# Kernel optimization log

Hardware: AMD Instinct MI355X
Metric: run time of the kernel (lower is better)

The kernel has to match this reference:

```python
import jax, jax.numpy as jnp
import numpy as np
from jax import lax

B, C, O, H, W = 4, 64, 64, 128, 128
K, PAD = 3, 1


def conv3x3(x, w, b):
    # standard 3x3 conv, stride 1, pad 1, NCHW / OIHW
    y = lax.conv_general_dilated(x, w, window_strides=(1, 1),
                                 padding=((PAD, PAD), (PAD, PAD)))
    return y + b[None, :, None, None]


def deform_conv(x, offset, w, b):
    # torchvision DeformConv2d (v1, 1 offset group): offset is [B, 2*K*K, H, W]
    # with (dy, dx) interleaved per kernel tap; sample pos = p0 + p_k + offset.
    Bn, Cn, Hn, Wn = x.shape
    off = offset.reshape(Bn, K * K, 2, Hn, Wn)
    ky, kx = jnp.meshgrid(jnp.arange(K), jnp.arange(K), indexing='ij')
    ky = ky.reshape(-1).astype(x.dtype)  # [9]
    kx = kx.reshape(-1).astype(x.dtype)
    base_y = jnp.arange(Hn, dtype=x.dtype)[None, None, :, None] - PAD + ky[None, :, None, None]
    base_x = jnp.arange(Wn, dtype=x.dtype)[None, None, None, :] - PAD + kx[None, :, None, None]
    py = base_y + off[:, :, 0]  # [B,9,H,W]
    px = base_x + off[:, :, 1]
    y0 = jnp.floor(py)
    x0 = jnp.floor(px)
    ly = py - y0  # bilinear fractional weights
    lx = px - x0
    y0i = y0.astype(jnp.int32)
    x0i = x0.astype(jnp.int32)
    xflat = x.reshape(Bn, Cn, Hn * Wn)

    def gather(yi, xi):
        valid = ((yi >= 0) & (yi < Hn) & (xi >= 0) & (xi < Wn)).astype(x.dtype)
        idx = (jnp.clip(yi, 0, Hn - 1) * Wn + jnp.clip(xi, 0, Wn - 1)).reshape(Bn, 1, -1)
        v = jnp.take_along_axis(xflat, idx, axis=2).reshape(Bn, Cn, K * K, Hn, Wn)
        return v * valid[:, None]  # zero padding outside image

    v00 = gather(y0i, x0i)
    v01 = gather(y0i, x0i + 1)
    v10 = gather(y0i + 1, x0i)
    v11 = gather(y0i + 1, x0i + 1)
    wy = ly[:, None]  # [B,1,9,H,W]
    wx = lx[:, None]
    samp = (v00 * (1 - wy) * (1 - wx) + v01 * (1 - wy) * wx
            + v10 * wy * (1 - wx) + v11 * wy * wx)  # [B,C,9,H,W]
    out = jnp.einsum('bckhw,ock->bohw', samp, w.reshape(w.shape[0], Cn, K * K))
    return out + b[None, :, None, None]


def setup_inputs() -> dict:
    key = jax.random.key(0)
    ks = jax.random.split(key, 16)
    n = lambda k, s, sc: jax.random.normal(k, s, jnp.float32) * sc
    inp = {
        'ref': n(ks[0], (B, C, H, W), 1.0),
        'nbr': n(ks[1], (B, C, H, W), 1.0),
        # offset convs: small weights so predicted offsets stay O(1) pixels
        'w_off1': n(ks[2], (18, 2 * C, 3, 3), 0.01), 'b_off1': n(ks[3], (18,), 0.01),
        'w_d1': n(ks[4], (O, C, 3, 3), 0.05), 'b_d1': n(ks[5], (O,), 0.05),
        'w_off2': n(ks[6], (18, 2 * O, 3, 3), 0.01), 'b_off2': n(ks[7], (18,), 0.01),
        'w_d2': n(ks[8], (O, O, 3, 3), 0.05), 'b_d2': n(ks[9], (O,), 0.05),
        'w_off3': n(ks[10], (18, 2 * O, 3, 3), 0.01), 'b_off3': n(ks[11], (18,), 0.01),
        'w_d3': n(ks[12], (O, O, 3, 3), 0.05), 'b_d3': n(ks[13], (O,), 0.05),
    }
    return inp


def reference(ref, nbr, w_off1, b_off1, w_d1, b_d1, w_off2, b_off2, w_d2, b_d2,
              w_off3, b_off3, w_d3, b_d3):
    offset1 = conv3x3(jnp.concatenate([ref, nbr], axis=1), w_off1, b_off1)
    d1 = deform_conv(nbr, offset1, w_d1, b_d1)
    offset2 = conv3x3(jnp.concatenate([ref, d1], axis=1), w_off2, b_off2)
    d2 = deform_conv(d1, offset2, w_d2, b_d2)
    offset3 = conv3x3(jnp.concatenate([ref, d2], axis=1), w_off3, b_off3)
    d3 = deform_conv(d2, offset3, w_d3, b_d3)
    return d3
```

## Files before the change

### kernel.cpp

```cpp
#include <hip/hip_runtime.h>
#include <hip/hip_bf16.h>

#define BB 4
#define CC 64
#define HH 128
#define WW 128
#define HW (HH * WW)
#define TOTPIX (BB * HW)

typedef short bf16x8 __attribute__((ext_vector_type(8)));
typedef float f32x4 __attribute__((ext_vector_type(4)));

static __device__ __forceinline__ short f2bf(float f) {
  __hip_bfloat16 h = __float2bfloat16(f);
  return __builtin_bit_cast(short, h);
}
static __device__ __forceinline__ float bf2f(short s) {
  unsigned int u = ((unsigned int)(unsigned short)s) << 16;
  return __builtin_bit_cast(float, u);
}

static __device__ __forceinline__ void stage1k(const short* g, short* lds) {
  __builtin_amdgcn_global_load_lds(
      (const __attribute__((address_space(1))) unsigned int*)g,
      (__attribute__((address_space(3))) unsigned int*)lds, 16, 0, 0);
}

__global__ __launch_bounds__(256) void cast_nhwc_kernel(
    const float* __restrict__ a, const float* __restrict__ b,
    short* __restrict__ oa, short* __restrict__ ob) {
  __shared__ float tile[64][68];
  const int bid = blockIdx.x;
  const int bb = bid >> 8;
  const int hw0 = (bid & 255) * 64;
  const int t = threadIdx.x;
  for (int s = 0; s < 2; s++) {
    const float* src = s ? b : a;
    short* dst = s ? ob : oa;
    if (s) __syncthreads();
    {
      const int lp = t & 15;
      for (int c = (t >> 4); c < 64; c += 16) {
        float4 v = *(const float4*)&src[((size_t)(bb * 64 + c)) * HW + hw0 + lp * 4];
        *(float4*)&tile[c][lp * 4] = v;
      }
    }
    __syncthreads();
    {
      const int px = t >> 2;
      const int seg = t & 3;
      bf16x8 s0, s1;
#pragma unroll
      for (int i = 0; i < 8; i++) s0[i] = f2bf(tile[seg * 16 + i][px]);
#pragma unroll
      for (int i = 0; i < 8; i++) s1[i] = f2bf(tile[seg * 16 + 8 + i][px]);
      short* dp = dst + ((size_t)(bid * 64 + px)) * 64 + seg * 16;
      *(bf16x8*)dp = s0;
      *(bf16x8*)(dp + 8) = s1;
    }
  }
}

__global__ __launch_bounds__(256) void prep_weights_all(
    const float* __restrict__ wd1, const float* __restrict__ wo1,
    short* __restrict__ wtd1, short* __restrict__ wtoff1,
    const float* __restrict__ wd2, const float* __restrict__ wo2,
    short* __restrict__ wtd2, short* __restrict__ wtoff2,
    const float* __restrict__ wd3, const float* __restrict__ wo3,
    short* __restrict__ wtd3, short* __restrict__ wtoff3) {
  const int s = blockIdx.x / 144;
  const float* wd = (s == 0) ? wd1 : (s == 1) ? wd2 : wd3;
  const float* wo = (s == 0) ? wo1 : (s == 1) ? wo2 : wo3;
  short* wtd = (s == 0) ? wtd1 : (s == 1) ? wtd2 : wtd3;
  short* wtoff = (s == 0) ? wtoff1 : (s == 1) ? wtoff2 : wtoff3;
  const int i = (blockIdx.x % 144) * 256 + threadIdx.x;
  const int j = i & 7, l = (i >> 3) & 63, f = i >> 9;
  {
    int ot = f & 3, cf = (f >> 2) & 1, k = f >> 3;
    int o = ot * 16 + (l & 15), c = cf * 32 + (l >> 4) * 8 + j;
    wtd[i] = f2bf(wd[(o * 64 + c) * 9 + k]);
  }
  {
    int ot = f & 1, ks = f >> 1;
    int cs = ks & 3, k = ks >> 2;
    int o = ot * 16 + (l & 15), c = cs * 32 + (l >> 4) * 8 + j;
    wtoff[i] = (o < 18) ? f2bf(wo[(o * 128 + c) * 9 + k]) : (short)0;
  }
}

__global__ __launch_bounds__(256, 4) void off_tile_kernel(
    const short* __restrict__ ref, const short* __restrict__ x2,
    const short* __restrict__ wtoff, const float* __restrict__ bias,
    float* __restrict__ out) {
  __shared__ short tile[2 * 6 * 24 * 64];
  int bid = blockIdx.x;
  bid = (bid & 7) * (gridDim.x >> 3) + (bid >> 3);
  const int tid = threadIdx.x;
  const int l = tid & 63;
  const int g = __builtin_amdgcn_readfirstlane(tid >> 6);
  const int col = l & 15, quad = l >> 4;
  const int b = bid >> 8;
  const int rem = bid & 255;
  const int h0 = (rem >> 3) * 4;
  const int w0 = (rem & 7) * 16;
  const int oy = h0 - 1, ox = w0 - 1;
  const int h = h0 + g, w = w0 + col;
  const int pix = ((b << 7) + h) * WW + w;

  const short* srcs[2] = {ref + (size_t)b * (HW * 64), x2 + (size_t)b * (HW * 64)};

  {
    const int tc = l >> 3;
    const int m = l & 7;
#pragma unroll
    for (int i = 0; i < 9; i++) {
      const int idx = g + i * 4;
      const int t = idx / 18;
      const int rr = (idx % 18) / 3, seg = idx % 3;
      const int iy = min(max(oy + rr, 0), HH - 1);
      const int tcol = seg * 8 + tc;
      const int ix = min(max(ox + tcol, 0), WW - 1);
      const int sc = (m - tcol) & 7;
      stage1k(srcs[t] + (((iy << 7) + ix) << 6) + sc * 8,
              &tile[((t * 6 + rr) * 24 + seg * 8) << 6]);
    }
  }

  f32x4 acc0 = {0.f, 0.f, 0.f, 0.f}, acc1 = {0.f, 0.f, 0.f, 0.f};
  const bf16x8* wp = (const bf16x8*)wtoff + l;

  __syncthreads();

#pragma unroll
  for (int k = 0; k < 9; k++) {
    const int ky = k / 3, kx = k - ky * 3;
    const int hh = h + ky - 1, ww2 = w + kx - 1;
    const bool valid = (hh >= 0) & (hh < HH) & (ww2 >= 0) & (ww2 < WW);
    const int tr = g + ky;
    const int tcx = col + kx;
#pragma unroll
    for (int cs = 0; cs < 4; cs++) {
      const int t = cs >> 1;
      const int chunk = (cs & 1) * 4 + quad;
      bf16x8 v = *(const bf16x8*)&tile[(((t * 6 + tr) * 24 + tcx) << 6) +
                                       (((chunk + tcx) & 7) << 3)];
      if (!valid) v = (bf16x8)(short)0;
      const int f = (k * 4 + cs) * 2;
      acc0 = __builtin_amdgcn_mfma_f32_16x16x32_bf16(wp[f * 64], v, acc0, 0, 0, 0);
      acc1 = __builtin_amdgcn_mfma_f32_16x16x32_bf16(wp[(f + 1) * 64], v, acc1, 0, 0, 0);
    }
  }

#pragma unroll
  for (int r = 0; r < 4; r++)
    out[(quad * 4 + r) * TOTPIX + pix] = acc0[r] + bias[quad * 4 + r];
  if (quad == 0) {
    out[16 * TOTPIX + pix] = acc1[0] + bias[16];
    out[17 * TOTPIX + pix] = acc1[1] + bias[17];
  }
}

#define TH 16
#define TWP 24
__global__ __launch_bounds__(512, 4) void deform_tile_kernel(
    const short* __restrict__ x, const float* __restrict__ off,
    const short* __restrict__ wtd, const float* __restrict__ bias,
    float* __restrict__ outf, short* __restrict__ outb) {
  __shared__ short tile[TH * TWP * 64];
  int bid = blockIdx.x;
  bid = (bid & 7) * (gridDim.x >> 3) + (bid >> 3);
  const int tid = threadIdx.x;
  const int l = tid & 63;
  const int wv = __builtin_amdgcn_readfirstlane(tid >> 6);
  const int col = l & 15, quad = l >> 4;
  const int b = bid >> 7;
  const int rem = bid & 127;
  const int h0 = (rem >> 3) * 8;
  const int w0 = (rem & 7) * 16;
  const int oy = h0 - 4, ox = w0 - 4;
  const int h = h0 + wv, w = w0 + col;
  const int pix = ((b << 7) + h) * WW + w;

  const short* xb = x + (size_t)b * (HW * 64);

  {
    const int tc = ((l >> 3) & 7);
    const int m = l & 7;
#pragma unroll
    for (int i = 0; i < 6; i++) {
      const int idx = wv + i * 8;
      const int r = idx / 3, seg = idx % 3;
      const int iy = min(max(oy + r, 0), HH - 1);
      const int tcol = seg * 8 + tc;
      const int ix = min(max(ox + tcol, 0), WW - 1);
      const int sc = (m - tcol) & 7;
      stage1k(xb + (((iy << 7) + ix) << 6) + sc * 8,
              &tile[((r * TWP + seg * 8) << 6)]);
    }
  }

  float offv[18];
#pragma unroll
  for (int j = 0; j < 18; j++) offv[j] = off[j * TOTPIX + pix];

  f32x4 acc[4];
#pragma unroll
  for (int ot = 0; ot < 4; ot++)
#pragma unroll
    for (int r = 0; r < 4; r++) acc[ot][r] = 0.f;

  const int c0g = quad * 8;
  const bf16x8* wp = (const bf16x8*)wtd + l;

  __syncthreads();

#pragma unroll
  for (int k = 0; k < 9; k++) {
    const int ky = k / 3, kx = k - ky * 3;
    const float py = (float)(h - 1 + ky) + offv[2 * k];
    const float pxx = (float)(w - 1 + kx) + offv[2 * k + 1];
    const float y0f = floorf(py), x0f = floorf(pxx);
    const float ly = py - y0f, lx = pxx - x0f;
    const int y0 = (int)y0f, x0 = (int)x0f;
    const int y1 = y0 + 1, x1 = x0 + 1;
    float w00 = (1.f - ly) * (1.f - lx), w01 = (1.f - ly) * lx;
    float w10 = ly * (1.f - lx), w11 = ly * lx;
    if (y0 < 0 || y0 >= HH) { w00 = 0.f; w01 = 0.f; }
    if (y1 < 0 || y1 >= HH) { w10 = 0.f; w11 = 0.f; }
    if (x0 < 0 || x0 >= WW) { w00 = 0.f; w10 = 0.f; }
    if (x1 < 0 || x1 >= WW) { w01 = 0.f; w11 = 0.f; }
    const int cy0 = min(max(y0, 0), HH - 1), cy1 = min(max(y1, 0), HH - 1);
    const int cx0 = min(max(x0, 0), WW - 1), cx1 = min(max(x1, 0), WW - 1);

    const int ty0 = cy0 - oy, ty1 = cy1 - oy;
    const int tx0 = cx0 - ox, tx1 = cx1 - ox;
    const bool intile = (ty0 >= 0) & (ty1 < TH) & (tx0 >= 0) & (tx1 < TWP);

    bf16x8 v00a, v00b, v01a, v01b, v10a, v10b, v11a, v11b;
    if (__builtin_amdgcn_ballot_w64(intile) == ~0ull) {
      const int p00 = ((ty0 * TWP + tx0) << 6);
      const int p01 = ((ty0 * TWP + tx1) << 6);
      const int p10 = ((ty1 * TWP + tx0) << 6);
      const int p11 = ((ty1 * TWP + tx1) << 6);
      v00a = *(const bf16x8*)&tile[p00 + (((quad + tx0) & 7) << 3)];
      v00b = *(const bf16x8*)&tile[p00 + (((quad + 4 + tx0) & 7) << 3)];
      v01a = *(const bf16x8*)&tile[p01 + (((quad + tx1) & 7) << 3)];
      v01b = *(const bf16x8*)&tile[p01 + (((quad + 4 + tx1) & 7) << 3)];
      v10a = *(const bf16x8*)&tile[p10 + (((quad + tx0) & 7) << 3)];
      v10b = *(const bf16x8*)&tile[p10 + (((quad + 4 + tx0) & 7) << 3)];
      v11a = *(const bf16x8*)&tile[p11 + (((quad + tx1) & 7) << 3)];
      v11b = *(const bf16x8*)&tile[p11 + (((quad + 4 + tx1) & 7) << 3)];
    } else {
      const int p00 = ((cy0 * WW + cx0) << 6) + c0g;
      const int p01 = ((cy0 * WW + cx1) << 6) + c0g;
      const int p10 = ((cy1 * WW + cx0) << 6) + c0g;
      const int p11 = ((cy1 * WW + cx1) << 6) + c0g;
      v00a = *(const bf16x8*)(xb + p00);
      v00b = *(const bf16x8*)(xb + p00 + 32);
      v01a = *(const bf16x8*)(xb + p01);
      v01b = *(const bf16x8*)(xb + p01 + 32);
      v10a = *(const bf16x8*)(xb + p10);
      v10b = *(const bf16x8*)(xb + p10 + 32);
      v11a = *(const bf16x8*)(xb + p11);
      v11b = *(const bf16x8*)(xb + p11 + 32);
    }

    bf16x8 bs0, bs1;
#pragma unroll
    for (int j = 0; j < 8; j++) {
      float sa = bf2f(v00a[j]) * w00 + bf2f(v01a[j]) * w01 +
                 bf2f(v10a[j]) * w10 + bf2f(v11a[j]) * w11;
      bs0[j] = f2bf(sa);
      float sb = bf2f(v00b[j]) * w00 + bf2f(v01b[j]) * w01 +
                 bf2f(v10b[j]) * w10 + bf2f(v11b[j]) * w11;
      bs1[j] = f2bf(sb);
    }

    acc[0] = __builtin_amdgcn_mfma_f32_16x16x32_bf16(wp[(k * 8 + 0) * 64], bs0, acc[0], 0, 0, 0);
    acc[1] = __builtin_amdgcn_mfma_f32_16x16x32_bf16(wp[(k * 8 + 1) * 64], bs0, acc[1], 0, 0, 0);
    acc[2] = __builtin_amdgcn_mfma_f32_16x16x32_bf16(wp[(k * 8 + 2) * 64], bs0, acc[2], 0, 0, 0);
    acc[3] = __builtin_amdgcn_mfma_f32_16x16x32_bf16(wp[(k * 8 + 3) * 64], bs0, acc[3], 0, 0, 0);
    acc[0] = __builtin_amdgcn_mfma_f32_16x16x32_bf16(wp[(k * 8 + 4) * 64], bs1, acc[0], 0, 0, 0);
    acc[1] = __builtin_amdgcn_mfma_f32_16x16x32_bf16(wp[(k * 8 + 5) * 64], bs1, acc[1], 0, 0, 0);
    acc[2] = __builtin_amdgcn_mfma_f32_16x16x32_bf16(wp[(k * 8 + 6) * 64], bs1, acc[2], 0, 0, 0);
    acc[3] = __builtin_amdgcn_mfma_f32_16x16x32_bf16(wp[(k * 8 + 7) * 64], bs1, acc[3], 0, 0, 0);
  }

#pragma unroll
  for (int ot = 0; ot < 4; ot++)
#pragma unroll
    for (int r = 0; r < 4; r++)
      acc[ot][r] += bias[ot * 16 + quad * 4 + r];

  if (outb) {
#pragma unroll
    for (int ot = 0; ot < 4; ot++) {
      short4 sv;
      sv.x = f2bf(acc[ot][0]); sv.y = f2bf(acc[ot][1]);
      sv.z = f2bf(acc[ot][2]); sv.w = f2bf(acc[ot][3]);
      *(short4*)(outb + (size_t)pix * 64 + ot * 16 + quad * 4) = sv;
    }
  }
  if (outf) {
    const int hw = pix & (HW - 1);
#pragma unroll
    for (int ot = 0; ot < 4; ot++)
#pragma unroll
      for (int r = 0; r < 4; r++) {
        const int o = ot * 16 + quad * 4 + r;
        outf[(size_t)b * (CC * HW) + (size_t)o * HW + hw] = acc[ot][r];
      }
  }
}

extern "C" void kernel_launch(void* const* d_in, const int* in_sizes, int n_in,
                              void* d_out, int out_size, void* d_ws, size_t ws_size,
                              hipStream_t stream) {
  const float* ref    = (const float*)d_in[0];
  const float* nbr    = (const float*)d_in[1];
  const float* w_off1 = (const float*)d_in[2];
  const float* b_off1 = (const float*)d_in[3];
  const float* w_d1   = (const float*)d_in[4];
  const float* b_d1   = (const float*)d_in[5];
  const float* w_off2 = (const float*)d_in[6];
  const float* b_off2 = (const float*)d_in[7];
  const float* w_d2   = (const float*)d_in[8];
  const float* b_d2   = (const float*)d_in[9];
  const float* w_off3 = (const float*)d_in[10];
  const float* b_off3 = (const float*)d_in[11];
  const float* w_d3   = (const float*)d_in[12];
  const float* b_d3   = (const float*)d_in[13];

  float* out = (float*)d_out;
  char* ws = (char*)d_ws;
  float* off_buf = (float*)(ws);
  short* ref_bf  = (short*)(ws + 5242880);
  short* nbr_bf  = (short*)(ws + 13631488);
  short* d1_bf   = (short*)(ws + 22020096);
  short* d2_bf   = (short*)(ws + 30408704);
  short* wtd1    = (short*)(ws + 38797312);
  short* wtd2    = (short*)(ws + 38871040);
  short* wtd3    = (short*)(ws + 38944768);
  short* wtoff1  = (short*)(ws + 39018496);
  short* wtoff2  = (short*)(ws + 39092224);
  short* wtoff3  = (short*)(ws + 39165952);

  cast_nhwc_kernel<<<1024, 256, 0, stream>>>(ref, nbr, ref_bf, nbr_bf);
  prep_weights_all<<<432, 256, 0, stream>>>(
      w_d1, w_off1, wtd1, wtoff1,
      w_d2, w_off2, wtd2, wtoff2,
      w_d3, w_off3, wtd3, wtoff3);

  const int nblk_oc = BB * HW / 64;
  const int nblk_df = BB * HW / 128;

  off_tile_kernel<<<nblk_oc, 256, 0, stream>>>(ref_bf, nbr_bf, wtoff1, b_off1, off_buf);
  deform_tile_kernel<<<nblk_df, 512, 0, stream>>>(nbr_bf, off_buf, wtd1, b_d1, nullptr, d1_bf);
  off_tile_kernel<<<nblk_oc, 256, 0, stream>>>(ref_bf, d1_bf, wtoff2, b_off2, off_buf);
  deform_tile_kernel<<<nblk_df, 512, 0, stream>>>(d1_bf, off_buf, wtd2, b_d2, nullptr, d2_bf);
  off_tile_kernel<<<nblk_oc, 256, 0, stream>>>(ref_bf, d2_bf, wtoff3, b_off3, off_buf);
  deform_tile_kernel<<<nblk_df, 512, 0, stream>>>(d2_bf, off_buf, wtd3, b_d3, out, nullptr);
}
```

Before: 120.8 us.

## Software-pipeline deform tap gathers with double-buffered registers ahead of blend and MFMA

Splits each kernel tap into a gather stage and a blend-plus-MFMA stage. The gathers for tap k+1 are issued before the tap k blend and MFMAs, with the two stages alternating between register sets A and B, and a sched_barrier keeps the compiler from merging them back. The aim is to hide LDS and global gather latency behind the interpolation and matrix work. This doubles the live gather registers, so the launch-bounds occupancy hint drops from 4 to 2 blocks to allow more VGPRs, at the risk of less latency hiding across waves.

```diff
diff --git a/kernel.cpp b/kernel.cpp
--- a/kernel.cpp
+++ b/kernel.cpp
@@ -162,7 +162,79 @@
 
 #define TH 16
 #define TWP 24
-__global__ __launch_bounds__(512, 4) void deform_tile_kernel(
+
+#define DST(k, S)                                                           \
+  {                                                                         \
+    const int ky = (k) / 3, kx = (k) - ky * 3;                              \
+    const float py = (float)(h - 1 + ky) + offv[2 * (k)];                   \
+    const float pxx = (float)(w - 1 + kx) + offv[2 * (k) + 1];              \
+    const float y0f = floorf(py), x0f = floorf(pxx);                        \
+    const float ly = py - y0f, lx = pxx - x0f;                              \
+    const int y0 = (int)y0f, x0 = (int)x0f;                                 \
+    const int y1 = y0 + 1, x1 = x0 + 1;                                     \
+    float w00 = (1.f - ly) * (1.f - lx), w01 = (1.f - ly) * lx;             \
+    float w10 = ly * (1.f - lx), w11 = ly * lx;                             \
+    if (y0 < 0 || y0 >= HH) { w00 = 0.f; w01 = 0.f; }                       \
+    if (y1 < 0 || y1 >= HH) { w10 = 0.f; w11 = 0.f; }                       \
+    if (x0 < 0 || x0 >= WW) { w00 = 0.f; w10 = 0.f; }                       \
+    if (x1 < 0 || x1 >= WW) { w01 = 0.f; w11 = 0.f; }                       \
+    const int cy0 = min(max(y0, 0), HH - 1), cy1 = min(max(y1, 0), HH - 1); \
+    const int cx0 = min(max(x0, 0), WW - 1), cx1 = min(max(x1, 0), WW - 1); \
+    const int ty0 = cy0 - oy, ty1 = cy1 - oy;                               \
+    const int tx0 = cx0 - ox, tx1 = cx1 - ox;                               \
+    const bool intile = (ty0 >= 0) & (ty1 < TH) & (tx0 >= 0) & (tx1 < TWP); \
+    if (__builtin_amdgcn_ballot_w64(intile) == ~0ull) {                     \
+      const int p00 = ((ty0 * TWP + tx0) << 6);                             \
+      const int p01 = ((ty0 * TWP + tx1) << 6);                             \
+      const int p10 = ((ty1 * TWP + tx0) << 6);                             \
+      const int p11 = ((ty1 * TWP + tx1) << 6);                             \
+      c##S##0 = *(const bf16x8*)&tile[p00 + (((quad + tx0) & 7) << 3)];     \
+      c##S##1 = *(const bf16x8*)&tile[p00 + (((quad + 4 + tx0) & 7) << 3)]; \
+      c##S##2 = *(const bf16x8*)&tile[p01 + (((quad + tx1) & 7) << 3)];     \
+      c##S##3 = *(const bf16x8*)&tile[p01 + (((quad + 4 + tx1) & 7) << 3)]; \
+      c##S##4 = *(const bf16x8*)&tile[p10 + (((quad + tx0) & 7) << 3)];     \
+      c##S##5 = *(const bf16x8*)&tile[p10 + (((quad + 4 + tx0) & 7) << 3)]; \
+      c##S##6 = *(const bf16x8*)&tile[p11 + (((quad + tx1) & 7) << 3)];     \
+      c##S##7 = *(const bf16x8*)&tile[p11 + (((quad + 4 + tx1) & 7) << 3)]; \
+    } else {                                                                \
+      const int p00 = ((cy0 * WW + cx0) << 6) + c0g;                        \
+      const int p01 = ((cy0 * WW + cx1) << 6) + c0g;                        \
+      const int p10 = ((cy1 * WW + cx0) << 6) + c0g;                        \
+      const int p11 = ((cy1 * WW + cx1) << 6) + c0g;                        \
+      c##S##0 = *(const bf16x8*)(xb + p00);                                 \
+      c##S##1 = *(const bf16x8*)(xb + p00 + 32);                            \
+      c##S##2 = *(const bf16x8*)(xb + p01);                                 \
+      c##S##3 = *(const bf16x8*)(xb + p01 + 32);                            \
+      c##S##4 = *(const bf16x8*)(xb + p10);                                 \
+      c##S##5 = *(const bf16x8*)(xb + p10 + 32);                            \
+      c##S##6 = *(const bf16x8*)(xb + p11);                                 \
+      c##S##7 = *(const bf16x8*)(xb + p11 + 32);                            \
+    }                                                                       \
+    sw##S##0 = w00; sw##S##1 = w01; sw##S##2 = w10; sw##S##3 = w11;         \
+  }
+
+#define DCP(k, S)                                                           \
+  {                                                                         \
+    bf16x8 bs0, bs1;                                                        \
+    _Pragma("unroll") for (int j = 0; j < 8; j++) {                         \
+      float sa = bf2f(c##S##0[j]) * sw##S##0 + bf2f(c##S##2[j]) * sw##S##1 +\
+                 bf2f(c##S##4[j]) * sw##S##2 + bf2f(c##S##6[j]) * sw##S##3; \
+      bs0[j] = f2bf(sa);                                                    \
+      float sb = bf2f(c##S##1[j]) * sw##S##0 + bf2f(c##S##3[j]) * sw##S##1 +\
+                 bf2f(c##S##5[j]) * sw##S##2 + bf2f(c##S##7[j]) * sw##S##3; \
+      bs1[j] = f2bf(sb);                                                    \
+    }                                                                       \
+    acc[0] = __builtin_amdgcn_mfma_f32_16x16x32_bf16(wp[((k) * 8 + 0) * 64], bs0, acc[0], 0, 0, 0); \
+    acc[1] = __builtin_amdgcn_mfma_f32_16x16x32_bf16(wp[((k) * 8 + 1) * 64], bs0, acc[1], 0, 0, 0); \
+    acc[2] = __builtin_amdgcn_mfma_f32_16x16x32_bf16(wp[((k) * 8 + 2) * 64], bs0, acc[2], 0, 0, 0); \
+    acc[3] = __builtin_amdgcn_mfma_f32_16x16x32_bf16(wp[((k) * 8 + 3) * 64], bs0, acc[3], 0, 0, 0); \
+    acc[0] = __builtin_amdgcn_mfma_f32_16x16x32_bf16(wp[((k) * 8 + 4) * 64], bs1, acc[0], 0, 0, 0); \
+    acc[1] = __builtin_amdgcn_mfma_f32_16x16x32_bf16(wp[((k) * 8 + 5) * 64], bs1, acc[1], 0, 0, 0); \
+    acc[2] = __builtin_amdgcn_mfma_f32_16x16x32_bf16(wp[((k) * 8 + 6) * 64], bs1, acc[2], 0, 0, 0); \
+    acc[3] = __builtin_amdgcn_mfma_f32_16x16x32_bf16(wp[((k) * 8 + 7) * 64], bs1, acc[3], 0, 0, 0); \
+  }
+
+__global__ __launch_bounds__(512, 2) void deform_tile_kernel(
     const short* __restrict__ x, const float* __restrict__ off,
     const short* __restrict__ wtd, const float* __restrict__ bias,
     float* __restrict__ outf, short* __restrict__ outb) {
@@ -212,78 +284,22 @@
   const int c0g = quad * 8;
   const bf16x8* wp = (const bf16x8*)wtd + l;
 
+  bf16x8 cA0, cA1, cA2, cA3, cA4, cA5, cA6, cA7;
+  bf16x8 cB0, cB1, cB2, cB3, cB4, cB5, cB6, cB7;
+  float swA0, swA1, swA2, swA3, swB0, swB1, swB2, swB3;
+
   __syncthreads();
 
+  DST(0, A)
 #pragma unroll
   for (int k = 0; k < 9; k++) {
-    const int ky = k / 3, kx = k - ky * 3;
-    const float py = (float)(h - 1 + ky) + offv[2 * k];
-    const float pxx = (float)(w - 1 + kx) + offv[2 * k + 1];
-    const float y0f = floorf(py), x0f = floorf(pxx);
-    const float ly = py - y0f, lx = pxx - x0f;
-    const int y0 = (int)y0f, x0 = (int)x0f;
-    const int y1 = y0 + 1, x1 = x0 + 1;
-    float w00 = (1.f - ly) * (1.f - lx), w01 = (1.f - ly) * lx;
-    float w10 = ly * (1.f - lx), w11 = ly * lx;
-    if (y0 < 0 || y0 >= HH) { w00 = 0.f; w01 = 0.f; }
-    if (y1 < 0 || y1 >= HH) { w10 = 0.f; w11 = 0.f; }
-    if (x0 < 0 || x0 >= WW) { w00 = 0.f; w10 = 0.f; }
-    if (x1 < 0 || x1 >= WW) { w01 = 0.f; w11 = 0.f; }
-    const int cy0 = min(max(y0, 0), HH - 1), cy1 = min(max(y1, 0), HH - 1);
-    const int cx0 = min(max(x0, 0), WW - 1), cx1 = min(max(x1, 0), WW - 1);
-
-    const int ty0 = cy0 - oy, ty1 = cy1 - oy;
-    const int tx0 = cx0 - ox, tx1 = cx1 - ox;
-    const bool intile = (ty0 >= 0) & (ty1 < TH) & (tx0 >= 0) & (tx1 < TWP);
-
-    bf16x8 v00a, v00b, v01a, v01b, v10a, v10b, v11a, v11b;
-    if (__builtin_amdgcn_ballot_w64(intile) == ~0ull) {
-      const int p00 = ((ty0 * TWP + tx0) << 6);
-      const int p01 = ((ty0 * TWP + tx1) << 6);
-      const int p10 = ((ty1 * TWP + tx0) << 6);
-      const int p11 = ((ty1 * TWP + tx1) << 6);
-      v00a = *(const bf16x8*)&tile[p00 + (((quad + tx0) & 7) << 3)];
-      v00b = *(const bf16x8*)&tile[p00 + (((quad + 4 + tx0) & 7) << 3)];
-      v01a = *(const bf16x8*)&tile[p01 + (((quad + tx1) & 7) << 3)];
-      v01b = *(const bf16x8*)&tile[p01 + (((quad + 4 + tx1) & 7) << 3)];
-      v10a = *(const bf16x8*)&tile[p10 + (((quad + tx0) & 7) << 3)];
-      v10b = *(const bf16x8*)&tile[p10 + (((quad + 4 + tx0) & 7) << 3)];
-      v11a = *(const bf16x8*)&tile[p11 + (((quad + tx1) & 7) << 3)];
-      v11b = *(const bf16x8*)&tile[p11 + (((quad + 4 + tx1) & 7) << 3)];
-    } else {
-      const int p00 = ((cy0 * WW + cx0) << 6) + c0g;
-      const int p01 = ((cy0 * WW + cx1) << 6) + c0g;
-      const int p10 = ((cy1 * WW + cx0) << 6) + c0g;
-      const int p11 = ((cy1 * WW + cx1) << 6) + c0g;
-      v00a = *(const bf16x8*)(xb + p00);
-      v00b = *(const bf16x8*)(xb + p00 + 32);
-      v01a = *(const bf16x8*)(xb + p01);
-      v01b = *(const bf16x8*)(xb + p01 + 32);
-      v10a = *(const bf16x8*)(xb + p10);
-      v10b = *(const bf16x8*)(xb + p10 + 32);
-      v11a = *(const bf16x8*)(xb + p11);
-      v11b = *(const bf16x8*)(xb + p11 + 32);
-    }
-
-    bf16x8 bs0, bs1;
-#pragma unroll
-    for (int j = 0; j < 8; j++) {
-      float sa = bf2f(v00a[j]) * w00 + bf2f(v01a[j]) * w01 +
-                 bf2f(v10a[j]) * w10 + bf2f(v11a[j]) * w11;
-      bs0[j] = f2bf(sa);
-      float sb = bf2f(v00b[j]) * w00 + bf2f(v01b[j]) * w01 +
-                 bf2f(v10b[j]) * w10 + bf2f(v11b[j]) * w11;
-      bs1[j] = f2bf(sb);
-    }
-
-    acc[0] = __builtin_amdgcn_mfma_f32_16x16x32_bf16(wp[(k * 8 + 0) * 64], bs0, acc[0], 0, 0, 0);
-    acc[1] = __builtin_amdgcn_mfma_f32_16x16x32_bf16(wp[(k * 8 + 1) * 64], bs0, acc[1], 0, 0, 0);
-    acc[2] = __builtin_amdgcn_mfma_f32_16x16x32_bf16(wp[(k * 8 + 2) * 64], bs0, acc[2], 0, 0, 0);
-    acc[3] = __builtin_amdgcn_mfma_f32_16x16x32_bf16(wp[(k * 8 + 3) * 64], bs0, acc[3], 0, 0, 0);
-    acc[0] = __builtin_amdgcn_mfma_f32_16x16x32_bf16(wp[(k * 8 + 4) * 64], bs1, acc[0], 0, 0, 0);
-    acc[1] = __builtin_amdgcn_mfma_f32_16x16x32_bf16(wp[(k * 8 + 5) * 64], bs1, acc[1], 0, 0, 0);
-    acc[2] = __builtin_amdgcn_mfma_f32_16x16x32_bf16(wp[(k * 8 + 6) * 64], bs1, acc[2], 0, 0, 0);
-    acc[3] = __builtin_amdgcn_mfma_f32_16x16x32_bf16(wp[(k * 8 + 7) * 64], bs1, acc[3], 0, 0, 0);
+    if (k < 8) {
+      if ((k & 1) == 0) { DST(k + 1, B) }
+      else              { DST(k + 1, A) }
+    }
+    __builtin_amdgcn_sched_barrier(0);
+    if ((k & 1) == 0) { DCP(k, A) }
+    else              { DCP(k, B) }
   }
 
 #pragma unroll
```

New measurement: 124.0 us. 2.7% more time.
